# Performance work log

Measured on AMD Instinct MI355X. Metric: run time of the kernel, lower is better.

The kernel has to match this reference:

```python
import jax, jax.numpy as jnp
import numpy as np
import math

B, L, D, H = 2, 1024, 1024, 16
HD = D // H          # 64
FFN = 2 * D          # 2048 (dim << 1 default)
TEMP = math.sqrt(HD)
EPS = 1e-5


def _layer_norm(x, g, b):
    m = jnp.mean(x, axis=-1, keepdims=True)
    v = jnp.mean(jnp.square(x - m), axis=-1, keepdims=True)
    return (x - m) * jax.lax.rsqrt(v + EPS) * g + b


def setup_inputs() -> dict:
    key = jax.random.key(0)
    ks = jax.random.split(key, 16)
    s = 0.02
    return {
        "x": jax.random.normal(ks[0], (B, L, D), jnp.float32),
        "edge_bias": jax.random.normal(ks[1], (B, L, L, H), jnp.float32),
        "padding_mask": jnp.zeros((B, L), dtype=bool),
        "wq": jax.random.normal(ks[2], (D, D), jnp.float32) * s,
        "wk": jax.random.normal(ks[3], (D, D), jnp.float32) * s,
        "wv": jax.random.normal(ks[4], (D, D), jnp.float32) * s,
        "wo": jax.random.normal(ks[5], (D, D), jnp.float32) * s,
        "bo": jnp.zeros((D,), jnp.float32),
        "wg": jax.random.normal(ks[6], (D, D), jnp.float32) * s,
        "bg": jnp.zeros((D,), jnp.float32),
        "w1": jax.random.normal(ks[7], (D, FFN), jnp.float32) * s,
        "b1": jnp.zeros((FFN,), jnp.float32),
        "w2": jax.random.normal(ks[8], (FFN, D), jnp.float32) * s,
        "b2": jnp.zeros((D,), jnp.float32),
        "ln1_g": jnp.ones((D,), jnp.float32),
        "ln1_b": jnp.zeros((D,), jnp.float32),
        "ln2_g": jnp.ones((D,), jnp.float32),
        "ln2_b": jnp.zeros((D,), jnp.float32),
    }


def reference(x, edge_bias, padding_mask, wq, wk, wv, wo, bo, wg, bg,
              w1, b1, w2, b2, ln1_g, ln1_b, ln2_g, ln2_b):
    # --- BiasedAttention (q = k = v = x) ---
    qh = (x @ wq).reshape(B, L, H, HD) / TEMP   # bqhd
    kh = (x @ wk).reshape(B, L, H, HD)          # bkhd
    vh = (x @ wv).reshape(B, L, H, HD)          # bkhd
    # scores in 'bkqh' layout, matching torch einsum('bqhd,bkhd->bkqh')
    attn = jnp.einsum('bqhd,bkhd->bkqh', qh, kh)
    attn = attn + jnp.transpose(edge_bias, (0, 2, 1, 3))  # bias is [b,q,k,h] -> [b,k,q,h]
    # key padding mask: masks entire key rows (axis 1 in bkqh)
    attn = jnp.where(padding_mask[:, :, None, None], -jnp.inf, attn)
    attn = jax.nn.softmax(attn, axis=1)  # softmax over keys
    o = jnp.einsum('bkqh,bkhd->bqhd', attn, vh).reshape(B, L, D)
    o = jax.nn.sigmoid(x @ wg + bg) * o          # sigmoid gate from raw q
    delta_x = o @ wo + bo
    attn_out = jnp.transpose(attn, (0, 2, 1, 3))  # [b,q,k,h]
    # --- residual + LN + FFN (eval mode: dropout/DropPath are identity) ---
    x = _layer_norm(x + delta_x, ln1_g, ln1_b)
    ffn = jax.nn.silu(x @ w1 + b1) @ w2 + b2
    x = _layer_norm(x + ffn, ln2_g, ln2_b)
    return (x, attn_out)
```

## Files before the change

### kernel.cpp

```cpp
#include <hip/hip_runtime.h>

typedef __bf16 bf16;
typedef _Float16 f16;
typedef bf16 bf16x8 __attribute__((ext_vector_type(8)));
typedef bf16 bf16x4 __attribute__((ext_vector_type(4)));
typedef f16 f16x4 __attribute__((ext_vector_type(4)));
typedef f16 f16x8 __attribute__((ext_vector_type(8)));
typedef float f32x4 __attribute__((ext_vector_type(4)));


__device__ __forceinline__ void gload16(const bf16* g, bf16* l) {
  __builtin_amdgcn_global_load_lds((const __attribute__((address_space(1))) unsigned int*)g,
                                   (__attribute__((address_space(3))) unsigned int*)l, 16, 0, 0);
}

__global__ __launch_bounds__(256) void kprep(
    const float* __restrict__ x, bf16* __restrict__ xbf,
    const float* __restrict__ wq, const float* __restrict__ wk, const float* __restrict__ wv,
    const float* __restrict__ wg, const float* __restrict__ wo, const float* __restrict__ w1,
    const float* __restrict__ w2, bf16* __restrict__ wqT, bf16* __restrict__ wkT,
    bf16* __restrict__ wvT, bf16* __restrict__ wgT, bf16* __restrict__ woT,
    bf16* __restrict__ w1T, bf16* __restrict__ w2T) {
  int bid = blockIdx.x;
  int tid = threadIdx.x;

  if (bid >= 9216) {
    int i = (bid - 9216) * 256 + tid;
    f32x4 v = *(const f32x4*)(x + (long)i * 4);
    bf16x4 o;
#pragma unroll
    for (int j = 0; j < 4; j++) o[j] = (bf16)v[j];
    *(bf16x4*)(xbf + (long)i * 4) = o;
    return;
  }

  __shared__ float t[32][33];
  const float* src;
  bf16* dst;
  int R, C, tile;
  if (bid < 5120) {
    int seg = bid >> 10;
    tile = bid & 1023;
    R = 1024; C = 1024;
    if (seg == 0) { src = wq; dst = wqT; }
    else if (seg == 1) { src = wk; dst = wkT; }
    else if (seg == 2) { src = wv; dst = wvT; }
    else if (seg == 3) { src = wg; dst = wgT; }
    else { src = wo; dst = woT; }
  } else if (bid < 7168) {
    tile = bid - 5120; R = 1024; C = 2048; src = w1; dst = w1T;
  } else {
    tile = bid - 7168; R = 2048; C = 1024; src = w2; dst = w2T;
  }
  int txs = (C == 2048) ? 6 : 5;
  int c0 = (tile & ((1 << txs) - 1)) << 5, r0 = (tile >> txs) << 5;
  int tx = tid & 31, ty = tid >> 5;
#pragma unroll
  for (int i = 0; i < 32; i += 8)
    t[ty + i][tx] = src[(long)(r0 + ty + i) * C + c0 + tx];
  __syncthreads();
#pragma unroll
  for (int i = 0; i < 32; i += 8)
    dst[(long)(c0 + ty + i) * R + r0 + tx] = (bf16)t[tx][ty + i];
}

static constexpr int MODE_QK = 0;
static constexpr int MODE_VT = 1;
static constexpr int MODE_G = 2;
static constexpr int MODE_SCOREF16 = 3;
static constexpr int MODE_SCORE_SC = 4;
static constexpr int MODE_PV = 5;
static constexpr int MODE_PV_SLOW = 6;
static constexpr int MODE_WO = 7;
static constexpr int MODE_FFN1 = 8;
static constexpr int MODE_FFN2 = 9;
static constexpr int MODE_QKVG = 10;

template <int MODE, int BN>
__global__ __launch_bounds__(256) void gemm_bt(
    const void* __restrict__ Av, const bf16* __restrict__ Bt, void* __restrict__ Out,
    const float* __restrict__ bias, const float* __restrict__ gate,
    int M, int N, int K, int lda, int ldb, long sA, long sB, float alpha) {
  const int z = blockIdx.z;
  const bf16* A = (const bf16*)Av + (long)z * sA;
  Bt += (long)z * sB;
  const int bb = z >> 4, hh = z & 15;

  constexpr int NT = (BN == 128) ? 4 : 2;
  __shared__ bf16 As[128 * 32];
  __shared__ bf16 Bs[BN * 32];

  const int tid = threadIdx.x;
  const int m0 = blockIdx.y * 128, n0 = blockIdx.x * BN;
  const int lane = tid & 63, wave = tid >> 6;
  const int wm = (wave >> 1) * 64;
  const int wn = (BN == 128) ? (wave & 1) * 64 : (wave & 1) * 32;
  const int l15 = lane & 15, quad = lane >> 4;

  const int srow = (lane >> 2);
  const int skc = (lane & 3) << 3;

  f32x4 acc[4][NT] = {};

  for (int k0 = 0; k0 < K; k0 += 32) {
    if (MODE == MODE_PV_SLOW) {
      bf16x8 av[2], bv;
#pragma unroll
      for (int u = 0; u < 2; u++) {
        int c = tid + u * 256;
        int row = c >> 2, kc = (c & 3) << 3;
        const float* Af = (const float*)Av;
        long rb = ((long)bb << 24) + hh + ((long)(m0 + row) << 14) + ((long)(k0 + kc) << 4);
#pragma unroll
        for (int j = 0; j < 8; j++) av[u][j] = (bf16)Af[rb + j * 16];
      }
      bv = *(const bf16x8*)(Bt + (long)(n0 + (tid >> 2)) * ldb + (k0 + ((tid & 3) << 3)));
      __syncthreads();
#pragma unroll
      for (int u = 0; u < 2; u++) {
        int c = tid + u * 256;
        *(bf16x8*)&As[c * 8] = av[u];
      }
      *(bf16x8*)&Bs[tid * 8] = bv;
    } else {
      __syncthreads();
      gload16(A + (long)(m0 + wave * 32 + srow) * lda + (k0 + skc), As + (wave * 2 + 0) * 512);
      gload16(A + (long)(m0 + wave * 32 + 16 + srow) * lda + (k0 + skc),
              As + (wave * 2 + 1) * 512);
      if (BN == 128) {
        gload16(Bt + (long)(n0 + wave * 32 + srow) * ldb + (k0 + skc), Bs + (wave * 2 + 0) * 512);
        gload16(Bt + (long)(n0 + wave * 32 + 16 + srow) * ldb + (k0 + skc),
                Bs + (wave * 2 + 1) * 512);
      } else {
        gload16(Bt + (long)(n0 + wave * 16 + srow) * ldb + (k0 + skc), Bs + wave * 512);
      }
    }
    __syncthreads();

    bf16x8 af[4], bfr[NT];
#pragma unroll
    for (int t = 0; t < 4; t++)
      af[t] = *(const bf16x8*)&As[(wm + t * 16 + l15) * 32 + (quad << 3)];
#pragma unroll
    for (int t = 0; t < NT; t++)
      bfr[t] = *(const bf16x8*)&Bs[(wn + t * 16 + l15) * 32 + (quad << 3)];
#pragma unroll
    for (int mt = 0; mt < 4; mt++)
#pragma unroll
      for (int nt = 0; nt < NT; nt++)
        acc[mt][nt] =
            __builtin_amdgcn_mfma_f32_16x16x32_bf16(af[mt], bfr[nt], acc[mt][nt], 0, 0, 0);
    if (MODE == MODE_PV_SLOW) __syncthreads();
  }

#pragma unroll
  for (int mt = 0; mt < 4; mt++) {
#pragma unroll
    for (int nt = 0; nt < NT; nt++) {
#pragma unroll
      for (int r = 0; r < 4; r++) {
        int m = m0 + wm + mt * 16 + (quad << 2) + r;
        int n = n0 + wn + nt * 16 + l15;
        float v = acc[mt][nt][r] * alpha;
        if (MODE == MODE_QK) {
          long off = ((long)((m >> 10) * 16 + (n >> 6)) * 1024 + (m & 1023)) * 64 + (n & 63);
          ((bf16*)Out)[off] = (bf16)v;
        } else if (MODE == MODE_VT) {
          long off = ((long)((m >> 10) * 16 + (n >> 6)) * 64 + (n & 63)) * 1024 + (m & 1023);
          ((bf16*)Out)[off] = (bf16)v;
        } else if (MODE == MODE_QKVG) {
          int sec = n >> 10, nn = n & 1023;
          bf16* ob = (bf16*)Out;
          if (sec == 0) {
            long off = ((long)((m >> 10) * 16 + (nn >> 6)) * 1024 + (m & 1023)) * 64 + (nn & 63);
            ob[off] = (bf16)(v * 0.125f);
          } else if (sec == 1) {
            long off = ((long)((m >> 10) * 16 + (nn >> 6)) * 1024 + (m & 1023)) * 64 + (nn & 63);
            (ob + 2097152)[off] = (bf16)v;
          } else if (sec == 2) {
            long off = ((long)((m >> 10) * 16 + (nn >> 6)) * 64 + (nn & 63)) * 1024 + (m & 1023);
            (ob + 4194304)[off] = (bf16)v;
          } else {
            float t = v + bias[nn];
            ((float*)(ob + 6291456))[(long)m * 1024 + nn] = 1.0f / (1.0f + __expf(-t));
          }
        } else if (MODE == MODE_SCOREF16) {
          ((f16*)Out)[((long)z << 20) + ((long)m << 10) + n] = (f16)v;
        } else if (MODE == MODE_SCORE_SC) {
          long off = ((long)bb << 24) + ((long)m << 14) + ((long)n << 4) + hh;
          ((float*)Out)[off] = v;
        } else if (MODE == MODE_PV || MODE == MODE_PV_SLOW) {
          long off = ((long)(bb * 1024 + m)) * 1024 + hh * 64 + n;
          ((bf16*)Out)[off] = (bf16)(v * gate[off]);
        } else if (MODE == MODE_WO) {
          ((float*)Out)[(long)m * N + n] = v + bias[n];
        } else if (MODE == MODE_FFN1) {
          float t = v + bias[n];
          ((bf16*)Out)[(long)m * N + n] = (bf16)(t / (1.0f + __expf(-t)));
        } else if (MODE == MODE_FFN2) {
          ((float*)Out)[(long)m * N + n] = v + bias[n];
        }
      }
    }
  }
}

__global__ __launch_bounds__(256, 4) void attn_softmax16(float* __restrict__ attnf,
                                                         void* __restrict__ Sf,
                                                         const float* __restrict__ ebias,
                                                         const unsigned char* __restrict__ mask) {
  __shared__ f16 sm[16][1032];
  int bx = blockIdx.x;
  int q = bx & 1023, b = bx >> 10;
  int tid = threadIdx.x;
  int lane = tid & 63, wave = tid >> 6;
  long sbase = ((long)b << 24) + ((long)q << 14);

  {
    int h = tid & 15;
    int kb = (tid >> 4) << 4;
#pragma unroll
    for (int it = 0; it < 4; it++) {
      int k0 = kb + it * 256;
      unsigned mw[4];
      *(uint4*)mw = *(const uint4*)(mask + (b << 10) + k0);
      f16 hv[16];
#pragma unroll
      for (int i = 0; i < 16; i++) {
        float v = ebias[sbase + (long)(k0 + i) * 16 + h];
        bool msk = (mw[i >> 2] >> ((i & 3) * 8)) & 255;
        hv[i] = msk ? (f16)(-60000.0f) : (f16)v;
      }
      *(f16x8*)&sm[h][k0] = *(f16x8*)&hv[0];
      *(f16x8*)&sm[h][k0 + 8] = *(f16x8*)&hv[8];
    }
  }

  f16* S = (f16*)Sf;
  f16x8 sv[4][2];
#pragma unroll
  for (int hi = 0; hi < 4; hi++) {
    int h = wave * 4 + hi;
    long srow = (((long)((b << 4) + h) << 10) + q) << 10;
    sv[hi][0] = *(const f16x8*)(S + srow + lane * 8);
    sv[hi][1] = *(const f16x8*)(S + srow + lane * 8 + 512);
  }
  __syncthreads();

#pragma unroll
  for (int hi = 0; hi < 4; hi++) {
    int h = wave * 4 + hi;
    long srow = (((long)((b << 4) + h) << 10) + q) << 10;
    f16x8 bv0 = *(const f16x8*)&sm[h][lane * 8];
    f16x8 bv1 = *(const f16x8*)&sm[h][lane * 8 + 512];
    float s_[16];
#pragma unroll
    for (int j = 0; j < 8; j++) {
      s_[j] = (float)sv[hi][0][j] + (float)bv0[j];
      s_[8 + j] = (float)sv[hi][1][j] + (float)bv1[j];
    }
    float mx = s_[0];
#pragma unroll
    for (int j = 1; j < 16; j++) mx = fmaxf(mx, s_[j]);
#pragma unroll
    for (int d = 32; d; d >>= 1) mx = fmaxf(mx, __shfl_xor(mx, d, 64));
    float sum = 0.f;
#pragma unroll
    for (int j = 0; j < 16; j++) {
      s_[j] = __expf(s_[j] - mx);
      sum += s_[j];
    }
#pragma unroll
    for (int d = 32; d; d >>= 1) sum += __shfl_xor(sum, d, 64);
    float inv = 1.0f / sum;
    bf16x8 pb0, pb1;
    f16 ph[16];
#pragma unroll
    for (int j = 0; j < 16; j++) {
      float pv = s_[j] * inv;
      ph[j] = (f16)pv;
      if (j < 8) pb0[j] = (bf16)pv; else pb1[j - 8] = (bf16)pv;
    }
    *(bf16x8*)((bf16*)Sf + srow + lane * 8) = pb0;
    *(bf16x8*)((bf16*)Sf + srow + lane * 8 + 512) = pb1;
    *(f16x8*)&sm[h][lane * 8] = *(f16x8*)&ph[0];
    *(f16x8*)&sm[h][lane * 8 + 512] = *(f16x8*)&ph[8];
  }
  __syncthreads();

#pragma unroll
  for (int it = 0; it < 16; it++) {
    int j = tid + it * 256;
    int k = j >> 2, c = (j & 3) << 2;
    f32x4 v;
#pragma unroll
    for (int jj = 0; jj < 4; jj++) v[jj] = (float)sm[c + jj][k];
    *(f32x4*)(attnf + sbase + ((long)k << 4) + c) = v;
  }
}

template <int FAST>
__global__ __launch_bounds__(256) void attn_softmax(float* __restrict__ attnf,
                                                    void* __restrict__ Sf,
                                                    const float* __restrict__ ebias,
                                                    const unsigned char* __restrict__ mask) {
  __shared__ float sm[8][1028];
  int bx = blockIdx.x;
  int hb = (bx & 1) * 8;
  int q = (bx >> 1) & 1023;
  int b = bx >> 11;
  int tid = threadIdx.x;
  int lane = tid & 63, wave = tid >> 6;
  long sbase = ((long)b << 24) + ((long)q << 14) + hb;

  for (int i = tid; i < 2048; i += 256) {
    int k = i >> 1, c = (i & 1) * 4;
    long off = sbase + ((long)k << 4) + c;
    f32x4 s = *(const f32x4*)(attnf + off);
    f32x4 e = *(const f32x4*)(ebias + off);
#pragma unroll
    for (int j = 0; j < 4; j++) sm[c + j][k] = s[j] + e[j];
  }
  __syncthreads();

  for (int k = tid; k < 1024; k += 256) {
    if (mask[(b << 10) + k]) {
#pragma unroll
      for (int h = 0; h < 8; h++) sm[h][k] = -1e30f;
    }
  }
  __syncthreads();

  for (int h = wave * 2; h < wave * 2 + 2; h++) {
    float mx = -1e30f;
    for (int k = lane; k < 1024; k += 64) mx = fmaxf(mx, sm[h][k]);
#pragma unroll
    for (int d = 32; d; d >>= 1) mx = fmaxf(mx, __shfl_xor(mx, d, 64));
    float sum = 0.f;
    for (int k = lane; k < 1024; k += 64) {
      float p = __expf(sm[h][k] - mx);
      sm[h][k] = p;
      sum += p;
    }
#pragma unroll
    for (int d = 32; d; d >>= 1) sum += __shfl_xor(sum, d, 64);
    float inv = 1.0f / sum;
    for (int k = lane; k < 1024; k += 64) sm[h][k] *= inv;
  }
  __syncthreads();

  for (int i = tid; i < 2048; i += 256) {
    int k = i >> 1, c = (i & 1) * 4;
    f32x4 v;
#pragma unroll
    for (int j = 0; j < 4; j++) v[j] = sm[c + j][k];
    *(f32x4*)(attnf + sbase + ((long)k << 4) + c) = v;
  }
}

template <int MODE>
__global__ __launch_bounds__(256) void layernorm_k(
    const float* __restrict__ a32, const float* __restrict__ b32, const float* __restrict__ g,
    const float* __restrict__ be, float* __restrict__ of32, bf16* __restrict__ obf) {
  __shared__ float red[8];
  long base = (long)blockIdx.x << 10;
  int tid = threadIdx.x;
  int lane = tid & 63, wave = tid >> 6;
  float h[4], sum = 0.f, sq = 0.f;
#pragma unroll
  for (int t = 0; t < 4; t++) {
    int i = tid + t * 256;
    float v = a32[base + i] + b32[base + i];
    h[t] = v;
    sum += v;
    sq += v * v;
  }
#pragma unroll
  for (int d = 32; d; d >>= 1) {
    sum += __shfl_xor(sum, d, 64);
    sq += __shfl_xor(sq, d, 64);
  }
  if (lane == 0) { red[wave] = sum; red[4 + wave] = sq; }
  __syncthreads();
  sum = red[0] + red[1] + red[2] + red[3];
  sq = red[4] + red[5] + red[6] + red[7];
  float mean = sum * (1.0f / 1024.0f);
  float var = sq * (1.0f / 1024.0f) - mean * mean;
  float rstd = rsqrtf(var + 1e-5f);
#pragma unroll
  for (int t = 0; t < 4; t++) {
    int i = tid + t * 256;
    float o = (h[t] - mean) * rstd * g[i] + be[i];
    of32[base + i] = o;
    if (MODE == 0) obf[base + i] = (bf16)o;
  }
}

extern "C" void kernel_launch(void* const* d_in, const int* in_sizes, int n_in, void* d_out,
                              int out_size, void* d_ws, size_t ws_size, hipStream_t stream) {
  const float* x = (const float*)d_in[0];
  const float* ebias = (const float*)d_in[1];
  const unsigned char* pmask = (const unsigned char*)d_in[2];
  const float* wq = (const float*)d_in[3];
  const float* wk = (const float*)d_in[4];
  const float* wv = (const float*)d_in[5];
  const float* wo = (const float*)d_in[6];
  const float* bo = (const float*)d_in[7];
  const float* wg = (const float*)d_in[8];
  const float* bg = (const float*)d_in[9];
  const float* w1 = (const float*)d_in[10];
  const float* b1 = (const float*)d_in[11];
  const float* w2 = (const float*)d_in[12];
  const float* b2 = (const float*)d_in[13];
  const float* ln1g = (const float*)d_in[14];
  const float* ln1b = (const float*)d_in[15];
  const float* ln2g = (const float*)d_in[16];
  const float* ln2b = (const float*)d_in[17];

  char* p = (char*)d_ws;
  bf16* xbf = (bf16*)p;  p += 4194304;
  bf16* wqT = (bf16*)p;  p += 2097152;
  bf16* wkT = (bf16*)p;  p += 2097152;
  bf16* wvT = (bf16*)p;  p += 2097152;
  bf16* wgT = (bf16*)p;  p += 2097152;
  bf16* woT = (bf16*)p;  p += 2097152;
  bf16* w1T = (bf16*)p;  p += 4194304;
  bf16* w2T = (bf16*)p;  p += 4194304;
  bf16* qws = (bf16*)p;  p += 4194304;
  bf16* kws = (bf16*)p;  p += 4194304;
  bf16* vtws = (bf16*)p; p += 4194304;
  float* gws = (float*)p; p += 8388608;
  bf16* ows = (bf16*)p;  p += 4194304;
  float* delta = (float*)p; p += 8388608;
  bf16* x1bf = (bf16*)p; p += 4194304;
  float* x1f = (float*)p; p += 8388608;
  bf16* ffn1 = (bf16*)p; p += 8388608;
  float* ffn2 = (float*)p; p += 8388608;
  size_t base_used = (size_t)(p - (char*)d_ws);
  void* Pws = (void*)p;
  bool fast = (base_used + 67108864ull) <= ws_size;
  (void)kws;

  float* xout = (float*)d_out;
  float* attnf = (float*)d_out + 2097152;

  dim3 blk(256);

  kprep<<<11264, blk, 0, stream>>>(x, xbf, wq, wk, wv, wg, wo, w1, w2, wqT, wkT, wvT, wgT, woT,
                                   w1T, w2T);

  gemm_bt<MODE_QKVG, 128><<<dim3(32, 16, 1), blk, 0, stream>>>(
      xbf, wqT, qws, bg, nullptr, 2048, 4096, 1024, 1024, 1024, 0, 0, 1.0f);

  if (fast) {
    gemm_bt<MODE_SCOREF16, 128><<<dim3(8, 8, 32), blk, 0, stream>>>(
        qws, kws, Pws, nullptr, nullptr, 1024, 1024, 64, 64, 64, 65536, 65536, 1.0f);
    attn_softmax16<<<2048, blk, 0, stream>>>(attnf, Pws, ebias, pmask);
    gemm_bt<MODE_PV, 64><<<dim3(1, 8, 32), blk, 0, stream>>>((bf16*)Pws, vtws, ows, nullptr, gws,
                                                             1024, 64, 1024, 1024, 1024, 1048576,
                                                             65536, 1.0f);
  } else {
    gemm_bt<MODE_SCORE_SC, 128><<<dim3(8, 8, 32), blk, 0, stream>>>(
        qws, kws, attnf, nullptr, nullptr, 1024, 1024, 64, 64, 64, 65536, 65536, 1.0f);
    attn_softmax<0><<<4096, blk, 0, stream>>>(attnf, nullptr, ebias, pmask);
    gemm_bt<MODE_PV_SLOW, 64><<<dim3(1, 8, 32), blk, 0, stream>>>(
        attnf, vtws, ows, nullptr, gws, 1024, 64, 1024, 1024, 1024, 0, 65536, 1.0f);
  }

  gemm_bt<MODE_WO, 64><<<dim3(16, 16, 1), blk, 0, stream>>>(ows, woT, delta, bo, nullptr, 2048,
                                                            1024, 1024, 1024, 1024, 0, 0, 1.0f);
  layernorm_k<0><<<2048, blk, 0, stream>>>(x, delta, ln1g, ln1b, x1f, x1bf);
  gemm_bt<MODE_FFN1, 128><<<dim3(16, 16, 1), blk, 0, stream>>>(x1bf, w1T, ffn1, b1, nullptr, 2048,
                                                               2048, 1024, 1024, 1024, 0, 0, 1.0f);
  gemm_bt<MODE_FFN2, 64><<<dim3(16, 16, 1), blk, 0, stream>>>(ffn1, w2T, ffn2, b2, nullptr, 2048,
                                                              1024, 2048, 2048, 2048, 0, 0, 1.0f);
  layernorm_k<1><<<2048, blk, 0, stream>>>(x1f, ffn2, ln2g, ln2b, xout, nullptr);
}
```

Measured before the change: 527.5 us.

## Split-K the Wo and FFN2 GEMMs, shrink GEMM tiles, widen softmax blocks

The Wo and FFN2 projections now run as two-way split-K GEMMs that write fp32 partial sums. The layernorm kernels add the two partials and the bias while fusing the residual. The QKVG and FFN1 GEMMs switch to 64-wide N tiles, and the attention softmax kernel uses 512-thread blocks with 2 heads per wave. The aim is more blocks in flight on small-grid GEMMs to fill the CUs, at the cost of extra partial-sum traffic and less per-block data reuse.

```diff
diff --git a/kernel.cpp b/kernel.cpp
--- a/kernel.cpp
+++ b/kernel.cpp
@@ -66,15 +66,13 @@
 
 static constexpr int MODE_QK = 0;
 static constexpr int MODE_VT = 1;
-static constexpr int MODE_G = 2;
 static constexpr int MODE_SCOREF16 = 3;
 static constexpr int MODE_SCORE_SC = 4;
 static constexpr int MODE_PV = 5;
 static constexpr int MODE_PV_SLOW = 6;
-static constexpr int MODE_WO = 7;
 static constexpr int MODE_FFN1 = 8;
-static constexpr int MODE_FFN2 = 9;
 static constexpr int MODE_QKVG = 10;
+static constexpr int MODE_PART = 11;
 
 template <int MODE, int BN>
 __global__ __launch_bounds__(256) void gemm_bt(
@@ -162,13 +160,7 @@
         int m = m0 + wm + mt * 16 + (quad << 2) + r;
         int n = n0 + wn + nt * 16 + l15;
         float v = acc[mt][nt][r] * alpha;
-        if (MODE == MODE_QK) {
-          long off = ((long)((m >> 10) * 16 + (n >> 6)) * 1024 + (m & 1023)) * 64 + (n & 63);
-          ((bf16*)Out)[off] = (bf16)v;
-        } else if (MODE == MODE_VT) {
-          long off = ((long)((m >> 10) * 16 + (n >> 6)) * 64 + (n & 63)) * 1024 + (m & 1023);
-          ((bf16*)Out)[off] = (bf16)v;
-        } else if (MODE == MODE_QKVG) {
+        if (MODE == MODE_QKVG) {
           int sec = n >> 10, nn = n & 1023;
           bf16* ob = (bf16*)Out;
           if (sec == 0) {
@@ -192,23 +184,21 @@
         } else if (MODE == MODE_PV || MODE == MODE_PV_SLOW) {
           long off = ((long)(bb * 1024 + m)) * 1024 + hh * 64 + n;
           ((bf16*)Out)[off] = (bf16)(v * gate[off]);
-        } else if (MODE == MODE_WO) {
-          ((float*)Out)[(long)m * N + n] = v + bias[n];
         } else if (MODE == MODE_FFN1) {
           float t = v + bias[n];
           ((bf16*)Out)[(long)m * N + n] = (bf16)(t / (1.0f + __expf(-t)));
-        } else if (MODE == MODE_FFN2) {
-          ((float*)Out)[(long)m * N + n] = v + bias[n];
+        } else if (MODE == MODE_PART) {
+          ((float*)Out)[((long)z << 21) + (long)m * N + n] = v;
         }
       }
     }
   }
 }
 
-__global__ __launch_bounds__(256, 4) void attn_softmax16(float* __restrict__ attnf,
-                                                         void* __restrict__ Sf,
-                                                         const float* __restrict__ ebias,
-                                                         const unsigned char* __restrict__ mask) {
+__global__ __launch_bounds__(512) void attn_softmax16(float* __restrict__ attnf,
+                                                      void* __restrict__ Sf,
+                                                      const float* __restrict__ ebias,
+                                                      const unsigned char* __restrict__ mask) {
   __shared__ f16 sm[16][1032];
   int bx = blockIdx.x;
   int q = bx & 1023, b = bx >> 10;
@@ -220,8 +210,8 @@
     int h = tid & 15;
     int kb = (tid >> 4) << 4;
 #pragma unroll
-    for (int it = 0; it < 4; it++) {
-      int k0 = kb + it * 256;
+    for (int it = 0; it < 2; it++) {
+      int k0 = kb + it * 512;
       unsigned mw[4];
       *(uint4*)mw = *(const uint4*)(mask + (b << 10) + k0);
       f16 hv[16];
@@ -237,10 +227,10 @@
   }
 
   f16* S = (f16*)Sf;
-  f16x8 sv[4][2];
-#pragma unroll
-  for (int hi = 0; hi < 4; hi++) {
-    int h = wave * 4 + hi;
+  f16x8 sv[2][2];
+#pragma unroll
+  for (int hi = 0; hi < 2; hi++) {
+    int h = wave * 2 + hi;
     long srow = (((long)((b << 4) + h) << 10) + q) << 10;
     sv[hi][0] = *(const f16x8*)(S + srow + lane * 8);
     sv[hi][1] = *(const f16x8*)(S + srow + lane * 8 + 512);
@@ -248,8 +238,8 @@
   __syncthreads();
 
 #pragma unroll
-  for (int hi = 0; hi < 4; hi++) {
-    int h = wave * 4 + hi;
+  for (int hi = 0; hi < 2; hi++) {
+    int h = wave * 2 + hi;
     long srow = (((long)((b << 4) + h) << 10) + q) << 10;
     f16x8 bv0 = *(const f16x8*)&sm[h][lane * 8];
     f16x8 bv1 = *(const f16x8*)&sm[h][lane * 8 + 512];
@@ -289,8 +279,8 @@
   __syncthreads();
 
 #pragma unroll
-  for (int it = 0; it < 16; it++) {
-    int j = tid + it * 256;
+  for (int it = 0; it < 8; it++) {
+    int j = tid + it * 512;
     int k = j >> 2, c = (j & 3) << 2;
     f32x4 v;
 #pragma unroll
@@ -360,8 +350,9 @@
 
 template <int MODE>
 __global__ __launch_bounds__(256) void layernorm_k(
-    const float* __restrict__ a32, const float* __restrict__ b32, const float* __restrict__ g,
-    const float* __restrict__ be, float* __restrict__ of32, bf16* __restrict__ obf) {
+    const float* __restrict__ a32, const float* __restrict__ b32, const float* __restrict__ c32,
+    const float* __restrict__ cb, const float* __restrict__ g, const float* __restrict__ be,
+    float* __restrict__ of32, bf16* __restrict__ obf) {
   __shared__ float red[8];
   long base = (long)blockIdx.x << 10;
   int tid = threadIdx.x;
@@ -370,7 +361,7 @@
 #pragma unroll
   for (int t = 0; t < 4; t++) {
     int i = tid + t * 256;
-    float v = a32[base + i] + b32[base + i];
+    float v = a32[base + i] + b32[base + i] + c32[base + i] + cb[i];
     h[t] = v;
     sum += v;
     sq += v * v;
@@ -431,11 +422,10 @@
   bf16* vtws = (bf16*)p; p += 4194304;
   float* gws = (float*)p; p += 8388608;
   bf16* ows = (bf16*)p;  p += 4194304;
-  float* delta = (float*)p; p += 8388608;
+  float* part = (float*)p; p += 16777216;
   bf16* x1bf = (bf16*)p; p += 4194304;
   float* x1f = (float*)p; p += 8388608;
   bf16* ffn1 = (bf16*)p; p += 8388608;
-  float* ffn2 = (float*)p; p += 8388608;
   size_t base_used = (size_t)(p - (char*)d_ws);
   void* Pws = (void*)p;
   bool fast = (base_used + 67108864ull) <= ws_size;
@@ -449,13 +439,13 @@
   kprep<<<11264, blk, 0, stream>>>(x, xbf, wq, wk, wv, wg, wo, w1, w2, wqT, wkT, wvT, wgT, woT,
                                    w1T, w2T);
 
-  gemm_bt<MODE_QKVG, 128><<<dim3(32, 16, 1), blk, 0, stream>>>(
+  gemm_bt<MODE_QKVG, 64><<<dim3(64, 16, 1), blk, 0, stream>>>(
       xbf, wqT, qws, bg, nullptr, 2048, 4096, 1024, 1024, 1024, 0, 0, 1.0f);
 
   if (fast) {
     gemm_bt<MODE_SCOREF16, 128><<<dim3(8, 8, 32), blk, 0, stream>>>(
         qws, kws, Pws, nullptr, nullptr, 1024, 1024, 64, 64, 64, 65536, 65536, 1.0f);
-    attn_softmax16<<<2048, blk, 0, stream>>>(attnf, Pws, ebias, pmask);
+    attn_softmax16<<<2048, dim3(512), 0, stream>>>(attnf, Pws, ebias, pmask);
     gemm_bt<MODE_PV, 64><<<dim3(1, 8, 32), blk, 0, stream>>>((bf16*)Pws, vtws, ows, nullptr, gws,
                                                              1024, 64, 1024, 1024, 1024, 1048576,
                                                              65536, 1.0f);
@@ -467,12 +457,13 @@
         attnf, vtws, ows, nullptr, gws, 1024, 64, 1024, 1024, 1024, 0, 65536, 1.0f);
   }
 
-  gemm_bt<MODE_WO, 64><<<dim3(16, 16, 1), blk, 0, stream>>>(ows, woT, delta, bo, nullptr, 2048,
-                                                            1024, 1024, 1024, 1024, 0, 0, 1.0f);
-  layernorm_k<0><<<2048, blk, 0, stream>>>(x, delta, ln1g, ln1b, x1f, x1bf);
-  gemm_bt<MODE_FFN1, 128><<<dim3(16, 16, 1), blk, 0, stream>>>(x1bf, w1T, ffn1, b1, nullptr, 2048,
-                                                               2048, 1024, 1024, 1024, 0, 0, 1.0f);
-  gemm_bt<MODE_FFN2, 64><<<dim3(16, 16, 1), blk, 0, stream>>>(ffn1, w2T, ffn2, b2, nullptr, 2048,
-                                                              1024, 2048, 2048, 2048, 0, 0, 1.0f);
-  layernorm_k<1><<<2048, blk, 0, stream>>>(x1f, ffn2, ln2g, ln2b, xout, nullptr);
-}
+  gemm_bt<MODE_PART, 64><<<dim3(16, 16, 2), blk, 0, stream>>>(
+      ows, woT, part, nullptr, nullptr, 2048, 1024, 512, 1024, 1024, 512, 512, 1.0f);
+  layernorm_k<0><<<2048, blk, 0, stream>>>(x, part, part + 2097152, bo, ln1g, ln1b, x1f, x1bf);
+  gemm_bt<MODE_FFN1, 64><<<dim3(32, 16, 1), blk, 0, stream>>>(
+      x1bf, w1T, ffn1, b1, nullptr, 2048, 2048, 1024, 1024, 1024, 0, 0, 1.0f);
+  gemm_bt<MODE_PART, 64><<<dim3(16, 16, 2), blk, 0, stream>>>(
+      ffn1, w2T, part, nullptr, nullptr, 2048, 1024, 1024, 2048, 2048, 1024, 1024, 1.0f);
+  layernorm_k<1><<<2048, blk, 0, stream>>>(x1f, part, part + 2097152, b2, ln2g, ln2b, xout,
+                                           nullptr);
+}
```

Measured after the change: 491.7 us. 1.07x faster.
